# Kernel tuning notes

Hardware: AMD Instinct MI355X
Metric: run time of the kernel (lower is better)

Reference implementation:

```python
import jax, jax.numpy as jnp
import numpy as np
import math

B, S, F, D = 8, 2048, 1024, 1024
NEG = -1e9


def setup_inputs() -> dict:
    key = jax.random.key(0)
    ks = jax.random.split(key, 5)
    x = jax.random.normal(ks[0], (B, S, F), dtype=jnp.float32)
    r_mat = jax.random.normal(ks[1], (B, S, S), dtype=jnp.float32)
    # shared causal attention mask [S, S] (1 = keep, 0 = masked)
    attn_mask = jnp.tril(jnp.ones((S, S), dtype=jnp.float32))
    # per-batch padding mask [B, 1, S]: last 128 tokens of half the batch padded
    pad = jnp.ones((B, 1, S), dtype=jnp.float32)
    pad = pad.at[B // 2:, :, S - 128:].set(0.0)
    Wq = jax.random.normal(ks[2], (F, D), dtype=jnp.float32) / math.sqrt(F)
    Wk = jax.random.normal(ks[3], (F, D), dtype=jnp.float32) / math.sqrt(F)
    Wv = jax.random.normal(ks[4], (F, D), dtype=jnp.float32) / math.sqrt(F)
    return {"x": x, "r_mat": r_mat, "attn_mask": attn_mask, "pad_mask": pad,
            "Wq": Wq, "Wk": Wk, "Wv": Wv}


def reference(x, r_mat, attn_mask, pad_mask, Wq, Wk, Wv):
    scale = math.sqrt(x.shape[-1])  # original scales by sqrt(features)
    q = jnp.einsum('bsf,fd->bsd', x, Wq)
    k = jnp.einsum('bsf,fd->bsd', x, Wk)
    v = jnp.einsum('bsf,fd->bsd', x, Wv)
    scores = jnp.einsum('bsd,btd->bst', q, k) / scale  # [B, S, S]
    keep = (pad_mask != 0.0) & (attn_mask[None] != 0.0)  # [B, S, S] broadcast
    r = jnp.where(keep, r_mat, NEG)
    r = jax.nn.softmax(r, axis=-1)
    scores = jnp.where(keep, scores + r, NEG)
    prob = jax.nn.softmax(scores, axis=-1)
    return jnp.einsum('bst,btd->bsd', prob, v)
```

## Files before the change

### kernel.cpp

```cpp
#include <hip/hip_runtime.h>
#include <hip/hip_bf16.h>

#define B_ 8
#define S_ 2048
#define F_ 1024
#define D_ 1024
#define TRI_ 136
#define TELEM_ 16384

typedef unsigned short u16;
typedef float f32x4 __attribute__((ext_vector_type(4)));
typedef __bf16 bf16x8 __attribute__((ext_vector_type(8)));
typedef unsigned short u16x8 __attribute__((ext_vector_type(8)));

__device__ __forceinline__ u16 f2bf(float f) {
  union { float f; unsigned u; } v; v.f = f;
  unsigned r = v.u + 0x7fff + ((v.u >> 16) & 1);
  return (u16)(r >> 16);
}
__device__ __forceinline__ float bf2f(u16 b) {
  union { unsigned u; float f; } v; v.u = ((unsigned)b) << 16;
  return v.f;
}

__device__ __forceinline__ void stage16(const u16* g, u16* l) {
  __builtin_amdgcn_global_load_lds(
      (const __attribute__((address_space(1))) void*)g,
      (__attribute__((address_space(3))) void*)l, 16, 0, 0);
}

__device__ __forceinline__ int xcd_swz(int f, int n) {
  int per = n >> 3;
  return (f & 7) * per + (f >> 3);
}


__global__ void cast_x(const float* __restrict__ x, u16* __restrict__ xb, int n4) {
  int i = blockIdx.x * blockDim.x + threadIdx.x;
  int stride = gridDim.x * blockDim.x;
  for (; i < n4; i += stride) {
    float4 v = ((const float4*)x)[i];
    ushort4 o;
    o.x = f2bf(v.x); o.y = f2bf(v.y); o.z = f2bf(v.z); o.w = f2bf(v.w);
    ((ushort4*)xb)[i] = o;
  }
}

__global__ void transW(const float* __restrict__ Wq, const float* __restrict__ Wk,
                       const float* __restrict__ Wv, u16* __restrict__ Wt) {
  __shared__ float tile[32][33];
  int z = blockIdx.z;
  const float* W = (z == 0) ? Wq : ((z == 1) ? Wk : Wv);
  int f0 = blockIdx.y * 32, d0 = blockIdx.x * 32;
  int tx = threadIdx.x & 31, ty = threadIdx.x >> 5;
  for (int i = 0; i < 4; i++)
    tile[ty + i * 8][tx] = W[(size_t)(f0 + ty + i * 8) * D_ + d0 + tx];
  __syncthreads();
  u16* o = Wt + (size_t)z * D_ * F_;
  for (int i = 0; i < 4; i++)
    o[(size_t)(d0 + ty + i * 8) * F_ + f0 + tx] = f2bf(tile[tx][ty + i * 8]);
}

__global__ __launch_bounds__(256) void er_pass(const float* __restrict__ r,
                                               const float* __restrict__ pm,
                                               u16* __restrict__ er,
                                               float* __restrict__ rs_r) {
  int row = blockIdx.x;
  int b = row >> 11, s = row & 2047;
  const float4* rp = (const float4*)(r + (size_t)row * S_);
  const float4* pp = (const float4*)(pm + (size_t)b * S_);
  int nk = (s >> 2) + 1;
  int nw = ((s >> 7) + 1) << 5;
  float4 ev[8];
  float acc = 0.f;
  #pragma unroll
  for (int it = 0; it < 8; it++) {
    int i = threadIdx.x + it * 256;
    if (i < nk) {
      float4 rv = rp[i], pv = pp[i];
      int t0 = i << 2;
      float4 e;
      #pragma unroll
      for (int j = 0; j < 4; j++) {
        bool keep = (t0 + j <= s) && ((&pv.x)[j] != 0.f);
        (&e.x)[j] = keep ? __expf((&rv.x)[j] - 16.f) : 0.f;
        acc += (&e.x)[j];
      }
      ev[it] = e;
    }
  }
  for (int off = 1; off < 64; off <<= 1) acc += __shfl_xor(acc, off);
  __shared__ float wsum[4];
  int lane = threadIdx.x & 63, w = threadIdx.x >> 6;
  if (lane == 0) wsum[w] = acc;
  __syncthreads();
  float total = wsum[0] + wsum[1] + wsum[2] + wsum[3];
  if (threadIdx.x == 0) rs_r[row] = total;
  float invr = 1.f / total;
  int c = s >> 7, rin = s & 127;
  u16* tb = er + (size_t)(b * TRI_ + c * (c + 1) / 2) * TELEM_ + rin * 128;
  #pragma unroll
  for (int it = 0; it < 8; it++) {
    int i = threadIdx.x + it * 256;
    if (i < nw) {
      int t0 = i << 2;
      float4 pv = pp[i];
      ushort4 o;
      #pragma unroll
      for (int j = 0; j < 4; j++) {
        bool keep = (t0 + j <= s) && ((&pv.x)[j] != 0.f);
        float val = keep ? (&ev[it].x)[j] * invr : -1e9f;
        (&o.x)[j] = f2bf(val);
      }
      *(ushort4*)(tb + (size_t)(t0 >> 7) * TELEM_ + (t0 & 127)) = o;
    }
  }
}

__global__ __launch_bounds__(256) void r_rowsum(const float* __restrict__ r,
                                                const float* __restrict__ pm,
                                                float* __restrict__ rs) {
  int row = blockIdx.x;
  int b = row >> 11, s = row & 2047;
  const float4* rp = (const float4*)(r + (size_t)row * S_);
  const float4* pp = (const float4*)(pm + (size_t)b * S_);
  int nv = (s >> 2) + 1;
  float acc = 0.f;
  for (int i = threadIdx.x; i < nv; i += 256) {
    float4 rv = rp[i];
    float4 pv = pp[i];
    int t0 = i << 2;
    #pragma unroll
    for (int j = 0; j < 4; j++) {
      int t = t0 + j;
      if (t <= s && (&pv.x)[j] != 0.f) acc += __expf((&rv.x)[j] - 16.f);
    }
  }
  for (int off = 1; off < 64; off <<= 1) acc += __shfl_xor(acc, off);
  __shared__ float wsum[4];
  int lane = threadIdx.x & 63, w = threadIdx.x >> 6;
  if (lane == 0) wsum[w] = acc;
  __syncthreads();
  if (threadIdx.x == 0) rs[row] = wsum[0] + wsum[1] + wsum[2] + wsum[3];
}


__device__ __forceinline__ bf16x8 readfrag(const u16* lds, int row, int ks, int hi) {
  int c = ((ks << 6) + (hi << 4)) ^ ((row & 7) << 4);
  return *(const bf16x8*)((const char*)lds + row * 128 + c);
}

#define SYNC_POINT()                                                             \
  __builtin_amdgcn_sched_barrier(0);                                             \
  __builtin_amdgcn_s_barrier();                                                  \
  __builtin_amdgcn_sched_barrier(0);


__device__ __forceinline__ void stageA(const u16* __restrict__ src, int ld, int h,
                                       u16* ldsA, int w, int l) {
  int base = ((w >> 2) * 128) + h * 64 + ((w & 3) * 16);
  int r = l >> 3, ch = (l & 7) ^ (l >> 3);
  #pragma unroll
  for (int i = 0; i < 2; i++) {
    int row = base + i * 8;
    stage16(src + (size_t)(row + r) * ld + ch * 8, ldsA + row * 64);
  }
}
__device__ __forceinline__ void stageB(const u16* __restrict__ src, int ld, int h,
                                       u16* ldsB, int w, int l) {
  int base = h * 128 + w * 16;
  int r = l >> 3, ch = (l & 7) ^ (l >> 3);
  #pragma unroll
  for (int i = 0; i < 2; i++) {
    int row = base + i * 8;
    stage16(src + (size_t)(row + r) * ld + ch * 8, ldsB + row * 64);
  }
}

#define MFMAQ(AF, KB, MB)                                                        \
  __builtin_amdgcn_s_setprio(1);                                                 \
  _Pragma("unroll")                                                              \
  for (int m = 0; m < 4; m++)                                                    \
    _Pragma("unroll")                                                            \
    for (int n = 0; n < 4; n++)                                                  \
      acc[(MB) + m][n] = __builtin_amdgcn_mfma_f32_16x16x32_bf16(                \
          AF[m], bfr[(KB) + n], acc[(MB) + m][n], 0, 0, 0);                      \
  __builtin_amdgcn_s_setprio(0);

__device__ __forceinline__ void gemm256(const u16* __restrict__ A, int lda,
                                        const u16* __restrict__ B, int ldb,
                                        int nT, u16* lds, f32x4 acc[8][4]) {
  const int t = threadIdx.x, w = t >> 6, l = t & 63;
  const int wr = w >> 2, wc = w & 3;
  u16* A0 = lds;           u16* B0 = lds + 16384;
  u16* A1 = lds + 32768;   u16* B1 = lds + 49152;

  #pragma unroll
  for (int m = 0; m < 8; m++)
    #pragma unroll
    for (int n = 0; n < 4; n++)
      #pragma unroll
      for (int j = 0; j < 4; j++) acc[m][n][j] = 0.f;

  stageB(B, ldb, 0, B0, w, l);
  stageB(B, ldb, 1, B0, w, l);
  stageA(A, lda, 0, A0, w, l);
  stageA(A, lda, 1, A0, w, l);
  if (nT > 1) stageA(A + 64, lda, 0, A1, w, l);
  asm volatile("s_waitcnt vmcnt(4)" ::: "memory");
  SYNC_POINT()

  const int arow = wr * 128 + (l & 15), brow = wc * 64 + (l & 15), hi = l >> 4;

  for (int kt = 0; kt < nT; kt++) {
    u16* cA = (kt & 1) ? A1 : A0;
    u16* cB = (kt & 1) ? B1 : B0;
    u16* nA = (kt & 1) ? A0 : A1;
    u16* nB = (kt & 1) ? B0 : B1;
    const u16* An1 = A + (size_t)(kt + 1) * 64;
    const u16* Bn1 = B + (size_t)(kt + 1) * 64;
    const u16* An2 = A + (size_t)(kt + 2) * 64;
    const bool has1 = (kt + 1 < nT), has2 = (kt + 2 < nT);
    bf16x8 af0[4], af1[4], bfr[8];

    #pragma unroll
    for (int m = 0; m < 4; m++) af0[m] = readfrag(cA, arow + m * 16, 0, hi);
    #pragma unroll
    for (int n = 0; n < 4; n++) bfr[n] = readfrag(cB, brow + n * 16, 0, hi);
    #pragma unroll
    for (int m = 0; m < 4; m++) af1[m] = readfrag(cA, arow + m * 16, 1, hi);
    #pragma unroll
    for (int n = 0; n < 4; n++) bfr[4 + n] = readfrag(cB, brow + n * 16, 1, hi);
    if (has1) stageB(Bn1, ldb, 0, nB, w, l);
    MFMAQ(af0, 0, 0)

    if (has1) {
      stageB(Bn1, ldb, 1, nB, w, l);
      asm volatile("s_waitcnt vmcnt(4)" ::: "memory");
    } else {
      asm volatile("s_waitcnt vmcnt(0)" ::: "memory");
    }
    SYNC_POINT()
    MFMAQ(af1, 4, 0)

    #pragma unroll
    for (int m = 0; m < 4; m++) af0[m] = readfrag(cA, arow + 64 + m * 16, 0, hi);
    #pragma unroll
    for (int m = 0; m < 4; m++) af1[m] = readfrag(cA, arow + 64 + m * 16, 1, hi);
    if (has2) stageA(An2, lda, 0, cA, w, l);
    MFMAQ(af0, 0, 4)

    if (has1) stageA(An1, lda, 1, nA, w, l);
    if (has1 && has2)  { asm volatile("s_waitcnt vmcnt(4)" ::: "memory"); }
    else if (has1)     { asm volatile("s_waitcnt vmcnt(2)" ::: "memory"); }
    else               { asm volatile("s_waitcnt vmcnt(0)" ::: "memory"); }
    SYNC_POINT()
    MFMAQ(af1, 4, 4)
  }
}

__device__ __forceinline__ void store256_bf16(f32x4 acc[8][4], u16* smem,
                                              u16* dst, int ld) {
  int t = threadIdx.x, w = t >> 6, l = t & 63;
  int wr = w >> 2, wc = w & 3;
  #pragma unroll
  for (int q = 0; q < 4; q++) {
    __syncthreads();
    if (wr == (q >> 1)) {
      int mb = (q & 1) * 4;
      #pragma unroll
      for (int mm = 0; mm < 4; mm++)
        #pragma unroll
        for (int j = 0; j < 4; j++) {
          int row = mm * 16 + (l >> 4) * 4 + j;
          #pragma unroll
          for (int n = 0; n < 4; n++)
            smem[row * 264 + wc * 64 + n * 16 + (l & 15)] = f2bf(acc[mb + mm][n][j]);
        }
    }
    __syncthreads();
    #pragma unroll
    for (int i = 0; i < 4; i++) {
      int idx = i * 512 + t;
      int row = idx >> 5, ch = idx & 31;
      *(u16x8*)(dst + (size_t)(q * 64 + row) * ld + ch * 8) =
          *(const u16x8*)(smem + row * 264 + ch * 8);
    }
  }
}

__global__ __launch_bounds__(512, 2) void gemm_qkv(
    const u16* __restrict__ xb, const u16* __restrict__ Wt,
    u16* __restrict__ qb, u16* __restrict__ kb, u16* __restrict__ vT) {
  __shared__ __align__(16) u16 lds[65536];
  int z = blockIdx.z;
  f32x4 acc[8][4];
  if (z < 2) {
    int m0 = blockIdx.x * 256, n0 = blockIdx.y * 256;
    gemm256(xb + (size_t)m0 * F_, F_,
            Wt + (size_t)z * D_ * F_ + (size_t)n0 * F_, F_, F_ / 64, lds, acc);
    store256_bf16(acc, lds, ((z == 0) ? qb : kb) + (size_t)m0 * D_ + n0, D_);
  } else {
    int d0 = blockIdx.y * 256, s0g = blockIdx.x * 256;
    gemm256(Wt + 2ULL * D_ * F_ + (size_t)d0 * F_, F_,
            xb + (size_t)s0g * F_, F_, F_ / 64, lds, acc);
    int b = s0g >> 11, s0 = s0g & 2047;
    store256_bf16(acc, lds, vT + (size_t)b * D_ * S_ + (size_t)d0 * S_ + s0, S_);
  }
}


template <int PACKA>
__device__ __forceinline__ void gemm128(const u16* __restrict__ A, int lda,
                                        const u16* __restrict__ B, int ldb,
                                        int nT, u16* lds, f32x4 acc[4][4]) {
  const int t = threadIdx.x, w = t >> 6, l = t & 63;
  const int wr = w >> 1, wc = w & 1;
  u16* A0 = lds;          u16* B0 = lds + 8192;
  u16* A1 = lds + 16384;  u16* B1 = lds + 24576;

  auto asrc = [&](int kt) -> const u16* {
    return PACKA ? A + (size_t)(kt >> 1) * TELEM_ + (kt & 1) * 64
                 : A + (size_t)kt * 64;
  };

  #pragma unroll
  for (int m = 0; m < 4; m++)
    #pragma unroll
    for (int n = 0; n < 4; n++)
      #pragma unroll
      for (int j = 0; j < 4; j++) acc[m][n][j] = 0.f;

  auto stg = [&](const u16* src, int ld, int h, u16* dst) {
    int base = h * 64 + w * 16;
    int r = l >> 3, ch = (l & 7) ^ (l >> 3);
    #pragma unroll
    for (int i = 0; i < 2; i++) {
      int row = base + i * 8;
      stage16(src + (size_t)(row + r) * ld + ch * 8, dst + row * 64);
    }
  };

  stg(asrc(0), PACKA ? 128 : lda, 0, A0);
  stg(asrc(0), PACKA ? 128 : lda, 1, A0);
  stg(B, ldb, 0, B0);
  stg(B, ldb, 1, B0);
  if (nT > 1) {
    stg(asrc(1), PACKA ? 128 : lda, 0, A1);
    stg(asrc(1), PACKA ? 128 : lda, 1, A1);
    asm volatile("s_waitcnt vmcnt(4)" ::: "memory");
  } else {
    asm volatile("s_waitcnt vmcnt(0)" ::: "memory");
  }
  SYNC_POINT()

  const int arow = wr * 64 + (l & 15), brow = wc * 64 + (l & 15), hi = l >> 4;

  for (int kt = 0; kt < nT; kt++) {
    u16* cA = (kt & 1) ? A1 : A0;
    u16* cB = (kt & 1) ? B1 : B0;
    u16* nB = (kt & 1) ? B0 : B1;
    const bool has1 = (kt + 1 < nT), has2 = (kt + 2 < nT);
    bf16x8 a0f[4], b0f[4], a1f[4], b1f[4];

    #pragma unroll
    for (int m = 0; m < 4; m++) a0f[m] = readfrag(cA, arow + m * 16, 0, hi);
    #pragma unroll
    for (int n = 0; n < 4; n++) b0f[n] = readfrag(cB, brow + n * 16, 0, hi);
    #pragma unroll
    for (int m = 0; m < 4; m++) a1f[m] = readfrag(cA, arow + m * 16, 1, hi);
    #pragma unroll
    for (int n = 0; n < 4; n++) b1f[n] = readfrag(cB, brow + n * 16, 1, hi);
    if (has1) {
      stg(B + (size_t)(kt + 1) * 64, ldb, 0, nB);
      stg(B + (size_t)(kt + 1) * 64, ldb, 1, nB);
    }
    __builtin_amdgcn_s_setprio(1);
    #pragma unroll
    for (int m = 0; m < 4; m++)
      #pragma unroll
      for (int n = 0; n < 4; n++)
        acc[m][n] = __builtin_amdgcn_mfma_f32_16x16x32_bf16(a0f[m], b0f[n], acc[m][n], 0, 0, 0);
    __builtin_amdgcn_s_setprio(0);
    asm volatile("s_waitcnt lgkmcnt(0)" ::: "memory");
    SYNC_POINT()

    if (has2) {
      stg(asrc(kt + 2), PACKA ? 128 : lda, 0, cA);
      stg(asrc(kt + 2), PACKA ? 128 : lda, 1, cA);
    }
    __builtin_amdgcn_s_setprio(1);
    #pragma unroll
    for (int m = 0; m < 4; m++)
      #pragma unroll
      for (int n = 0; n < 4; n++)
        acc[m][n] = __builtin_amdgcn_mfma_f32_16x16x32_bf16(a1f[m], b1f[n], acc[m][n], 0, 0, 0);
    __builtin_amdgcn_s_setprio(0);
    if (has2)      { asm volatile("s_waitcnt vmcnt(4)" ::: "memory"); }
    else if (has1) { asm volatile("s_waitcnt vmcnt(0)" ::: "memory"); }
    SYNC_POINT()
  }
}

__device__ __forceinline__ void tri_decode(int x, int& mt, int& nt) {
  mt = (int)((sqrtf(8.f * x + 1.f) - 1.f) * 0.5f);
  while ((mt + 1) * (mt + 2) / 2 <= x) mt++;
  while (mt * (mt + 1) / 2 > x) mt--;
  nt = x - mt * (mt + 1) / 2;
}

__global__ __launch_bounds__(256, 2) void attn_scores_er(
    const u16* __restrict__ qb, const u16* __restrict__ kb,
    const u16* __restrict__ er, u16* __restrict__ P,
    float* __restrict__ rowsum) {
  __shared__ __align__(16) u16 lds[32768];
  int f = xcd_swz(blockIdx.x + 136 * blockIdx.y, 1088);
  int x = f % 136, b = f / 136;
  int mt, nt; tri_decode(x, mt, nt);
  int m0 = mt * 128, n0 = nt * 128;
  f32x4 acc[4][4];
  gemm128<0>(qb + ((size_t)b * S_ + m0) * D_, D_,
             kb + ((size_t)b * S_ + n0) * D_, D_, D_ / 64, lds, acc);
  int t = threadIdx.x, w = t >> 6, l = t & 63;
  int wr = w >> 1, wc = w & 1;
  float* fs = (float*)lds;
  size_t tbase = (size_t)(b * TRI_ + mt * (mt + 1) / 2 + nt) * TELEM_;
  #pragma unroll
  for (int h = 0; h < 2; h++) {
    __syncthreads();
    if (wr == h) {
      #pragma unroll
      for (int m = 0; m < 4; m++)
        #pragma unroll
        for (int j = 0; j < 4; j++) {
          int row = m * 16 + (l >> 4) * 4 + j;
          #pragma unroll
          for (int n = 0; n < 4; n++)
            fs[row * 132 + wc * 64 + n * 16 + (l & 15)] = acc[m][n][j];
        }
    }
    __syncthreads();
    int row = t >> 2, cg = t & 3;
    int rin = h * 64 + row;
    const u16* et = er + tbase + (size_t)rin * 128 + cg * 32;
    u16* pt = P + tbase + (size_t)rin * 128 + cg * 32;
    const float* fsc = fs + row * 132 + cg * 32;
    float rsum = 0.f;
    #pragma unroll
    for (int cc = 0; cc < 4; cc++) {
      int ch = (cg + cc) & 3;
      f32x4 q0 = *(const f32x4*)(fsc + ch * 8);
      f32x4 q1 = *(const f32x4*)(fsc + ch * 8 + 4);
      u16x8 e8 = *(const u16x8*)(et + ch * 8);
      u16x8 o;
      #pragma unroll
      for (int k = 0; k < 8; k++) {
        float qk = (k < 4) ? q0[k] : q1[k - 4];
        float e = __expf(fmaf(qk, 0.03125f, bf2f(e8[k]) - 16.f));
        u16 pb = f2bf(e); o[k] = pb; rsum += bf2f(pb);
      }
      *(u16x8*)(pt + ch * 8) = o;
    }
    rsum += __shfl_xor(rsum, 1);
    rsum += __shfl_xor(rsum, 2);
    if ((t & 3) == 0) atomicAdd(&rowsum[b * S_ + m0 + rin], rsum);
  }
}

__global__ __launch_bounds__(256, 2) void attn_scores_rm(
    const u16* __restrict__ qb, const u16* __restrict__ kb,
    const float* __restrict__ r_mat, const float* __restrict__ pm,
    const float* __restrict__ rs_r, u16* __restrict__ P,
    float* __restrict__ rowsum) {
  __shared__ __align__(16) u16 lds[32768];
  int f = xcd_swz(blockIdx.x + 136 * blockIdx.y, 1088);
  int x = f % 136, b = f / 136;
  int mt, nt; tri_decode(x, mt, nt);
  int m0 = mt * 128, n0 = nt * 128;
  f32x4 acc[4][4];
  gemm128<0>(qb + ((size_t)b * S_ + m0) * D_, D_,
             kb + ((size_t)b * S_ + n0) * D_, D_, D_ / 64, lds, acc);
  int t = threadIdx.x, w = t >> 6, l = t & 63;
  int wr = w >> 1, wc = w & 1;
  float* fs = (float*)lds;
  const float* rb = r_mat + (size_t)b * S_ * S_;
  const float* pmp = pm + (size_t)b * S_ + n0;
  size_t tbase = (size_t)(b * TRI_ + mt * (mt + 1) / 2 + nt) * TELEM_;
  #pragma unroll
  for (int h = 0; h < 2; h++) {
    __syncthreads();
    if (wr == h) {
      #pragma unroll
      for (int m = 0; m < 4; m++)
        #pragma unroll
        for (int j = 0; j < 4; j++) {
          int row = m * 16 + (l >> 4) * 4 + j;
          #pragma unroll
          for (int n = 0; n < 4; n++)
            fs[row * 132 + wc * 64 + n * 16 + (l & 15)] = acc[m][n][j];
        }
    }
    __syncthreads();
    int row = t >> 2, cg = t & 3;
    int srow = m0 + h * 64 + row;
    float invr = 1.f / rs_r[b * S_ + srow];
    const float* rrow = rb + (size_t)srow * S_ + n0 + cg * 32;
    u16* pt = P + tbase + (size_t)(h * 64 + row) * 128 + cg * 32;
    const float* fsc = fs + row * 132 + cg * 32;
    float rsum = 0.f;
    #pragma unroll
    for (int cc = 0; cc < 4; cc++) {
      int ch = (cg + cc) & 3;
      f32x4 q0 = *(const f32x4*)(fsc + ch * 8);
      f32x4 q1 = *(const f32x4*)(fsc + ch * 8 + 4);
      f32x4 r0 = *(const f32x4*)(rrow + ch * 8);
      f32x4 r1 = *(const f32x4*)(rrow + ch * 8 + 4);
      f32x4 p0 = *(const f32x4*)(pmp + cg * 32 + ch * 8);
      f32x4 p1 = *(const f32x4*)(pmp + cg * 32 + ch * 8 + 4);
      u16x8 o;
      #pragma unroll
      for (int k = 0; k < 8; k++) {
        int tc = n0 + cg * 32 + ch * 8 + k;
        float rv = (k < 4) ? r0[k] : r1[k - 4];
        float pmv = (k < 4) ? p0[k] : p1[k - 4];
        float qk = (k < 4) ? q0[k] : q1[k - 4];
        bool keep = (tc <= srow) && (pmv != 0.f);
        float rsm = __expf(rv - 16.f) * invr;
        float e = keep ? __expf(fmaf(qk, 0.03125f, rsm - 16.f)) : 0.f;
        u16 pb = f2bf(e); o[k] = pb; rsum += bf2f(pb);
      }
      *(u16x8*)(pt + ch * 8) = o;
    }
    rsum += __shfl_xor(rsum, 1);
    rsum += __shfl_xor(rsum, 2);
    if ((t & 3) == 0) atomicAdd(&rowsum[b * S_ + srow], rsum);
  }
}

__global__ __launch_bounds__(256, 2) void attn_pv(
    const u16* __restrict__ P, const u16* __restrict__ vT,
    const float* __restrict__ rowsum, float* __restrict__ out) {
  __shared__ __align__(16) u16 lds[32768];
  int f = xcd_swz(blockIdx.x + 16 * blockIdx.y + 128 * blockIdx.z, 1024);
  int mt = 15 - (f & 15), dt = (f >> 4) & 7, b = f >> 7;
  int m0 = mt * 128, n0 = dt * 128;
  int nT = 2 * (mt + 1);
  f32x4 acc[4][4];
  gemm128<1>(P + (size_t)(b * TRI_ + mt * (mt + 1) / 2) * TELEM_, 128,
             vT + ((size_t)b * D_ + n0) * S_, S_, nT, lds, acc);
  int t = threadIdx.x, w = t >> 6, l = t & 63;
  int wr = w >> 1, wc = w & 1;
  float* fs = (float*)lds;
  #pragma unroll
  for (int h = 0; h < 2; h++) {
    __syncthreads();
    if (wr == h) {
      #pragma unroll
      for (int m = 0; m < 4; m++)
        #pragma unroll
        for (int j = 0; j < 4; j++) {
          int row = m * 16 + (l >> 4) * 4 + j;
          float inv = 1.f / rowsum[b * S_ + m0 + h * 64 + row];
          #pragma unroll
          for (int n = 0; n < 4; n++)
            fs[row * 132 + wc * 64 + n * 16 + (l & 15)] = acc[m][n][j] * inv;
        }
    }
    __syncthreads();
    #pragma unroll
    for (int i = 0; i < 8; i++) {
      int idx = i * 256 + t;
      int row = idx >> 5, c4 = (idx & 31) << 2;
      *(float4*)(out + ((size_t)b * S_ + m0 + h * 64 + row) * D_ + n0 + c4) =
          *(const float4*)(fs + row * 132 + c4);
    }
  }
}

extern "C" void kernel_launch(void* const* d_in, const int* in_sizes, int n_in,
                              void* d_out, int out_size, void* d_ws, size_t ws_size,
                              hipStream_t stream) {
  const float* x     = (const float*)d_in[0];
  const float* r_mat = (const float*)d_in[1];
  const float* pm    = (const float*)d_in[3];
  const float* Wq    = (const float*)d_in[4];
  const float* Wk    = (const float*)d_in[5];
  const float* Wv    = (const float*)d_in[6];
  float* out = (float*)d_out;
  char* ws = (char*)d_ws;

  const size_t PK = (size_t)B_ * TRI_ * TELEM_ * 2;
  u16*   qb     = (u16*)(ws + 0);
  u16*   kb     = (u16*)(ws + 33554432ULL);
  u16*   vT     = (u16*)(ws + 67108864ULL);
  float* rowsum = (float*)(ws + 100663296ULL);
  float* rs_r   = (float*)(ws + 100728832ULL);
  u16*   xb     = (u16*)(ws + 100794368ULL);
  u16*   Wt     = (u16*)(ws + 134348800ULL);
  u16*   er     = (u16*)(ws + 100794368ULL);
  bool use_er   = ws_size >= 100794368ULL + 2 * PK;
  u16*   P      = use_er ? (u16*)(ws + 100794368ULL + PK)
                         : (u16*)(ws + 100794368ULL);

  cast_x<<<dim3(2048), dim3(256), 0, stream>>>(x, xb, (B_ * S_ * F_) / 4);
  transW<<<dim3(32, 32, 3), dim3(256), 0, stream>>>(Wq, Wk, Wv, Wt);
  if (!use_er)
    r_rowsum<<<dim3(B_ * S_), dim3(256), 0, stream>>>(r_mat, pm, rs_r);
  gemm_qkv<<<dim3(64, 4, 3), dim3(512), 0, stream>>>(xb, Wt, qb, kb, vT);
  hipMemsetAsync(rowsum, 0, B_ * S_ * sizeof(float), stream);
  if (use_er) {
    er_pass<<<dim3(B_ * S_), dim3(256), 0, stream>>>(r_mat, pm, er, rs_r);
    attn_scores_er<<<dim3(136, 8), dim3(256), 0, stream>>>(qb, kb, er, P, rowsum);
  } else {
    attn_scores_rm<<<dim3(136, 8), dim3(256), 0, stream>>>(qb, kb, r_mat, pm, rs_r, P, rowsum);
  }
  attn_pv<<<dim3(16, 8, 8), dim3(256), 0, stream>>>(P, vT, rowsum, out);
}
```

Baseline: 274.0 us.

## Load GEMM B operand directly to registers, fuse prep kernels and drop memset

The QKV GEMM now loads the B operand straight from global memory into register fragments, double-buffered in registers, instead of staging it through LDS. This halves LDS usage to allow more occupancy and removes the LDS round trip for B. The cast and weight-transpose kernels are merged into one launch, and the rowsum memset is folded into er_pass on the default path, cutting launch overhead. In exchange the GEMM main loop now waits for vmcnt(0) every tile, and the direct B loads are uncoalesced 16-byte reads from global memory.

```diff
diff --git a/kernel.cpp b/kernel.cpp
--- a/kernel.cpp
+++ b/kernel.cpp
@@ -35,38 +35,44 @@
 }
 
 
-__global__ void cast_x(const float* __restrict__ x, u16* __restrict__ xb, int n4) {
-  int i = blockIdx.x * blockDim.x + threadIdx.x;
-  int stride = gridDim.x * blockDim.x;
-  for (; i < n4; i += stride) {
-    float4 v = ((const float4*)x)[i];
-    ushort4 o;
-    o.x = f2bf(v.x); o.y = f2bf(v.y); o.z = f2bf(v.z); o.w = f2bf(v.w);
-    ((ushort4*)xb)[i] = o;
-  }
-}
-
-__global__ void transW(const float* __restrict__ Wq, const float* __restrict__ Wk,
-                       const float* __restrict__ Wv, u16* __restrict__ Wt) {
+__global__ __launch_bounds__(256) void prep(const float* __restrict__ x,
+                                            const float* __restrict__ Wq,
+                                            const float* __restrict__ Wk,
+                                            const float* __restrict__ Wv,
+                                            u16* __restrict__ xb,
+                                            u16* __restrict__ Wt) {
   __shared__ float tile[32][33];
-  int z = blockIdx.z;
-  const float* W = (z == 0) ? Wq : ((z == 1) ? Wk : Wv);
-  int f0 = blockIdx.y * 32, d0 = blockIdx.x * 32;
-  int tx = threadIdx.x & 31, ty = threadIdx.x >> 5;
-  for (int i = 0; i < 4; i++)
-    tile[ty + i * 8][tx] = W[(size_t)(f0 + ty + i * 8) * D_ + d0 + tx];
-  __syncthreads();
-  u16* o = Wt + (size_t)z * D_ * F_;
-  for (int i = 0; i < 4; i++)
-    o[(size_t)(d0 + ty + i * 8) * F_ + f0 + tx] = f2bf(tile[tx][ty + i * 8]);
+  if (blockIdx.x < 2048) {
+    int n4 = (B_ * S_ * F_) / 4;
+    for (int i = blockIdx.x * 256 + threadIdx.x; i < n4; i += 2048 * 256) {
+      float4 v = ((const float4*)x)[i];
+      ushort4 o;
+      o.x = f2bf(v.x); o.y = f2bf(v.y); o.z = f2bf(v.z); o.w = f2bf(v.w);
+      ((ushort4*)xb)[i] = o;
+    }
+  } else {
+    int f = blockIdx.x - 2048;
+    int z = f >> 10;
+    int f2 = f & 1023;
+    int f0 = (f2 >> 5) * 32, d0 = (f2 & 31) * 32;
+    const float* W = (z == 0) ? Wq : ((z == 1) ? Wk : Wv);
+    int tx = threadIdx.x & 31, ty = threadIdx.x >> 5;
+    for (int i = 0; i < 4; i++)
+      tile[ty + i * 8][tx] = W[(size_t)(f0 + ty + i * 8) * D_ + d0 + tx];
+    __syncthreads();
+    u16* o = Wt + (size_t)z * D_ * F_;
+    for (int i = 0; i < 4; i++)
+      o[(size_t)(d0 + ty + i * 8) * F_ + f0 + tx] = f2bf(tile[tx][ty + i * 8]);
+  }
 }
 
 __global__ __launch_bounds__(256) void er_pass(const float* __restrict__ r,
                                                const float* __restrict__ pm,
                                                u16* __restrict__ er,
-                                               float* __restrict__ rs_r) {
+                                               float* __restrict__ rowsum) {
   int row = blockIdx.x;
   int b = row >> 11, s = row & 2047;
+  if (threadIdx.x == 0) rowsum[row] = 0.f;
   const float4* rp = (const float4*)(r + (size_t)row * S_);
   const float4* pp = (const float4*)(pm + (size_t)b * S_);
   int nk = (s >> 2) + 1;
@@ -94,9 +100,7 @@
   int lane = threadIdx.x & 63, w = threadIdx.x >> 6;
   if (lane == 0) wsum[w] = acc;
   __syncthreads();
-  float total = wsum[0] + wsum[1] + wsum[2] + wsum[3];
-  if (threadIdx.x == 0) rs_r[row] = total;
-  float invr = 1.f / total;
+  float invr = 1.f / (wsum[0] + wsum[1] + wsum[2] + wsum[3]);
   int c = s >> 7, rin = s & 127;
   u16* tb = er + (size_t)(b * TRI_ + c * (c + 1) / 2) * TELEM_ + rin * 128;
   #pragma unroll
@@ -166,34 +170,54 @@
     stage16(src + (size_t)(row + r) * ld + ch * 8, ldsA + row * 64);
   }
 }
-__device__ __forceinline__ void stageB(const u16* __restrict__ src, int ld, int h,
-                                       u16* ldsB, int w, int l) {
-  int base = h * 128 + w * 16;
-  int r = l >> 3, ch = (l & 7) ^ (l >> 3);
-  #pragma unroll
-  for (int i = 0; i < 2; i++) {
-    int row = base + i * 8;
-    stage16(src + (size_t)(row + r) * ld + ch * 8, ldsB + row * 64);
-  }
-}
-
-#define MFMAQ(AF, KB, MB)                                                        \
+
+#define BLOAD(DST, KT)                                                           \
+  _Pragma("unroll")                                                              \
+  for (int n = 0; n < 4; n++) {                                                  \
+    DST[n]     = *(const bf16x8*)(bb + (size_t)n * 16 * ldb + (KT) * 64);        \
+    DST[4 + n] = *(const bf16x8*)(bb + (size_t)n * 16 * ldb + (KT) * 64 + 32);   \
+  }
+
+#define MFMAQ2(AF, BQ, KB, MB)                                                   \
   __builtin_amdgcn_s_setprio(1);                                                 \
   _Pragma("unroll")                                                              \
   for (int m = 0; m < 4; m++)                                                    \
     _Pragma("unroll")                                                            \
     for (int n = 0; n < 4; n++)                                                  \
       acc[(MB) + m][n] = __builtin_amdgcn_mfma_f32_16x16x32_bf16(                \
-          AF[m], bfr[(KB) + n], acc[(MB) + m][n], 0, 0, 0);                      \
+          AF[m], BQ[(KB) + n], acc[(MB) + m][n], 0, 0, 0);                       \
   __builtin_amdgcn_s_setprio(0);
 
+#define TILE256(KT, CU, NX, BQ, BN)                                              \
+  {                                                                              \
+    const bool h1 = (KT) + 1 < nT;                                               \
+    bf16x8 af0[4], af1[4];                                                       \
+    _Pragma("unroll")                                                            \
+    for (int m = 0; m < 4; m++) af0[m] = readfrag(CU, arow + m * 16, 0, hi);     \
+    _Pragma("unroll")                                                            \
+    for (int m = 0; m < 4; m++) af1[m] = readfrag(CU, arow + m * 16, 1, hi);     \
+    if (h1) { BLOAD(BN, (KT) + 1) }                                              \
+    if (h1) stageA(A + (size_t)((KT) + 1) * 64, lda, 0, NX, w, l);               \
+    MFMAQ2(af0, BQ, 0, 0)                                                        \
+    if (h1) stageA(A + (size_t)((KT) + 1) * 64, lda, 1, NX, w, l);               \
+    MFMAQ2(af1, BQ, 4, 0)                                                        \
+    _Pragma("unroll")                                                            \
+    for (int m = 0; m < 4; m++) af0[m] = readfrag(CU, arow + 64 + m * 16, 0, hi);\
+    _Pragma("unroll")                                                            \
+    for (int m = 0; m < 4; m++) af1[m] = readfrag(CU, arow + 64 + m * 16, 1, hi);\
+    MFMAQ2(af0, BQ, 0, 4)                                                        \
+    MFMAQ2(af1, BQ, 4, 4)                                                        \
+    asm volatile("s_waitcnt vmcnt(0)" ::: "memory");                             \
+    SYNC_POINT()                                                                 \
+  }
+
 __device__ __forceinline__ void gemm256(const u16* __restrict__ A, int lda,
-                                        const u16* __restrict__ B, int ldb,
+                                        const u16* __restrict__ Bg, int ldb,
                                         int nT, u16* lds, f32x4 acc[8][4]) {
   const int t = threadIdx.x, w = t >> 6, l = t & 63;
   const int wr = w >> 2, wc = w & 3;
-  u16* A0 = lds;           u16* B0 = lds + 16384;
-  u16* A1 = lds + 32768;   u16* B1 = lds + 49152;
+  u16* A0 = lds;
+  u16* A1 = lds + 16384;
 
   #pragma unroll
   for (int m = 0; m < 8; m++)
@@ -202,60 +226,22 @@
       #pragma unroll
       for (int j = 0; j < 4; j++) acc[m][n][j] = 0.f;
 
-  stageB(B, ldb, 0, B0, w, l);
-  stageB(B, ldb, 1, B0, w, l);
+  const u16* bb = Bg + (size_t)(wc * 64 + (l & 15)) * ldb + (l >> 4) * 8;
+  bf16x8 bqE[8], bqO[8];
+
   stageA(A, lda, 0, A0, w, l);
   stageA(A, lda, 1, A0, w, l);
-  if (nT > 1) stageA(A + 64, lda, 0, A1, w, l);
-  asm volatile("s_waitcnt vmcnt(4)" ::: "memory");
+  BLOAD(bqE, 0)
+  asm volatile("s_waitcnt vmcnt(0)" ::: "memory");
   SYNC_POINT()
 
-  const int arow = wr * 128 + (l & 15), brow = wc * 64 + (l & 15), hi = l >> 4;
-
-  for (int kt = 0; kt < nT; kt++) {
-    u16* cA = (kt & 1) ? A1 : A0;
-    u16* cB = (kt & 1) ? B1 : B0;
-    u16* nA = (kt & 1) ? A0 : A1;
-    u16* nB = (kt & 1) ? B0 : B1;
-    const u16* An1 = A + (size_t)(kt + 1) * 64;
-    const u16* Bn1 = B + (size_t)(kt + 1) * 64;
-    const u16* An2 = A + (size_t)(kt + 2) * 64;
-    const bool has1 = (kt + 1 < nT), has2 = (kt + 2 < nT);
-    bf16x8 af0[4], af1[4], bfr[8];
-
-    #pragma unroll
-    for (int m = 0; m < 4; m++) af0[m] = readfrag(cA, arow + m * 16, 0, hi);
-    #pragma unroll
-    for (int n = 0; n < 4; n++) bfr[n] = readfrag(cB, brow + n * 16, 0, hi);
-    #pragma unroll
-    for (int m = 0; m < 4; m++) af1[m] = readfrag(cA, arow + m * 16, 1, hi);
-    #pragma unroll
-    for (int n = 0; n < 4; n++) bfr[4 + n] = readfrag(cB, brow + n * 16, 1, hi);
-    if (has1) stageB(Bn1, ldb, 0, nB, w, l);
-    MFMAQ(af0, 0, 0)
-
-    if (has1) {
-      stageB(Bn1, ldb, 1, nB, w, l);
-      asm volatile("s_waitcnt vmcnt(4)" ::: "memory");
-    } else {
-      asm volatile("s_waitcnt vmcnt(0)" ::: "memory");
-    }
-    SYNC_POINT()
-    MFMAQ(af1, 4, 0)
-
-    #pragma unroll
-    for (int m = 0; m < 4; m++) af0[m] = readfrag(cA, arow + 64 + m * 16, 0, hi);
-    #pragma unroll
-    for (int m = 0; m < 4; m++) af1[m] = readfrag(cA, arow + 64 + m * 16, 1, hi);
-    if (has2) stageA(An2, lda, 0, cA, w, l);
-    MFMAQ(af0, 0, 4)
-
-    if (has1) stageA(An1, lda, 1, nA, w, l);
-    if (has1 && has2)  { asm volatile("s_waitcnt vmcnt(4)" ::: "memory"); }
-    else if (has1)     { asm volatile("s_waitcnt vmcnt(2)" ::: "memory"); }
-    else               { asm volatile("s_waitcnt vmcnt(0)" ::: "memory"); }
-    SYNC_POINT()
-    MFMAQ(af1, 4, 4)
+  const int arow = wr * 128 + (l & 15), hi = l >> 4;
+
+  for (int kt2 = 0; kt2 < nT; kt2 += 2) {
+    TILE256(kt2, A0, A1, bqE, bqO)
+    if (kt2 + 1 < nT) {
+      TILE256(kt2 + 1, A1, A0, bqO, bqE)
+    }
   }
 }
 
@@ -292,7 +278,7 @@
 __global__ __launch_bounds__(512, 2) void gemm_qkv(
     const u16* __restrict__ xb, const u16* __restrict__ Wt,
     u16* __restrict__ qb, u16* __restrict__ kb, u16* __restrict__ vT) {
-  __shared__ __align__(16) u16 lds[65536];
+  __shared__ __align__(16) u16 lds[33792];
   int z = blockIdx.z;
   f32x4 acc[8][4];
   if (z < 2) {
@@ -602,16 +588,15 @@
   u16*   P      = use_er ? (u16*)(ws + 100794368ULL + PK)
                          : (u16*)(ws + 100794368ULL);
 
-  cast_x<<<dim3(2048), dim3(256), 0, stream>>>(x, xb, (B_ * S_ * F_) / 4);
-  transW<<<dim3(32, 32, 3), dim3(256), 0, stream>>>(Wq, Wk, Wv, Wt);
+  prep<<<dim3(5120), dim3(256), 0, stream>>>(x, Wq, Wk, Wv, xb, Wt);
   if (!use_er)
     r_rowsum<<<dim3(B_ * S_), dim3(256), 0, stream>>>(r_mat, pm, rs_r);
   gemm_qkv<<<dim3(64, 4, 3), dim3(512), 0, stream>>>(xb, Wt, qb, kb, vT);
-  hipMemsetAsync(rowsum, 0, B_ * S_ * sizeof(float), stream);
   if (use_er) {
-    er_pass<<<dim3(B_ * S_), dim3(256), 0, stream>>>(r_mat, pm, er, rs_r);
+    er_pass<<<dim3(B_ * S_), dim3(256), 0, stream>>>(r_mat, pm, er, rowsum);
     attn_scores_er<<<dim3(136, 8), dim3(256), 0, stream>>>(qb, kb, er, P, rowsum);
   } else {
+    hipMemsetAsync(rowsum, 0, B_ * S_ * sizeof(float), stream);
     attn_scores_rm<<<dim3(136, 8), dim3(256), 0, stream>>>(qb, kb, r_mat, pm, rs_r, P, rowsum);
   }
   attn_pv<<<dim3(16, 8, 8), dim3(256), 0, stream>>>(P, vT, rowsum, out);
```

After: 393.4 us. 1.44x slower.
